# Kernel tuning notes

Hardware: AMD Instinct MI355X
Metric: run time of the kernel (lower is better)

The kernel has to match this reference:

```python
import jax, jax.numpy as jnp
import numpy as np

N, E, DIN, DOUT = 30000, 480000, 512, 512


def setup_inputs() -> dict:
    key = jax.random.key(0)
    ks = jax.random.split(key, 20)
    inp = {}
    inp["x"] = jax.random.normal(ks[0], (N, DIN), jnp.float32)
    inp["edge_index"] = jax.random.randint(ks[1], (2, E), 0, N, dtype=jnp.int64)
    inp["edge_weight"] = jax.random.uniform(ks[2], (E,), jnp.float32)
    sc = 1.0 / np.sqrt(DIN)
    sl = 1.0 / np.sqrt(2 * DOUT)
    for i, g in enumerate(["i", "f", "g", "o"]):
        inp[f"Wc_{g}"] = jax.random.normal(ks[3 + 4 * i], (DIN, DOUT), jnp.float32) * sc
        inp[f"bc_{g}"] = jnp.zeros((DOUT,), jnp.float32)
        inp[f"Wl_{g}"] = jax.random.normal(ks[4 + 4 * i], (2 * DOUT, DOUT), jnp.float32) * sl
        inp[f"bl_{g}"] = jnp.zeros((DOUT,), jnp.float32)
    return inp


def _gcn_norm(src, dst, w, n):
    # add self loops with weight 1.0 (improved=False), then symmetric normalization
    loops = jnp.arange(n, dtype=src.dtype)
    src = jnp.concatenate([src, loops])
    dst = jnp.concatenate([dst, loops])
    w = jnp.concatenate([w, jnp.ones((n,), w.dtype)])
    deg = jax.ops.segment_sum(w, dst, num_segments=n)
    dinv = jnp.where(deg > 0, jax.lax.rsqrt(jnp.where(deg > 0, deg, 1.0)), 0.0)
    norm = dinv[src] * w * dinv[dst]
    return src, dst, norm


def reference(x, edge_index, edge_weight,
              Wc_i, bc_i, Wl_i, bl_i,
              Wc_f, bc_f, Wl_f, bl_f,
              Wc_g, bc_g, Wl_g, bl_g,
              Wc_o, bc_o, Wl_o, bl_o):
    n = x.shape[0]
    src, dst, norm = _gcn_norm(edge_index[0], edge_index[1], edge_weight, n)
    H = jnp.zeros((n, DOUT), x.dtype)  # _set_hidden_state default
    C = jnp.zeros((n, DOUT), x.dtype)  # _set_cell_state default

    def conv(Wc, bc):
        xw = x @ Wc                                        # [N, DOUT] dense GEMM
        agg = jax.ops.segment_sum(norm[:, None] * xw[src], dst, num_segments=n)
        return agg + bc

    def gate(Wc, bc, Wl, bl, act):
        z = jnp.concatenate([conv(Wc, bc), H], axis=1)      # [N, 2*DOUT]
        return act(z @ Wl + bl)

    I = gate(Wc_i, bc_i, Wl_i, bl_i, jax.nn.sigmoid)
    F = gate(Wc_f, bc_f, Wl_f, bl_f, jax.nn.sigmoid)
    G = gate(Wc_g, bc_g, Wl_g, bl_g, jnp.tanh)
    O = gate(Wc_o, bc_o, Wl_o, bl_o, jax.nn.sigmoid)
    Cn = F * C + I * G
    Hn = O * jnp.tanh(Cn)
    return O, Hn, Cn
```

## Files before the change

kernel.cpp:

```cpp
#include <hip/hip_runtime.h>
#include <stdint.h>

typedef __bf16 bf16;
typedef __attribute__((ext_vector_type(4))) float f4;
typedef __attribute__((ext_vector_type(4))) float f32x4;
typedef __attribute__((ext_vector_type(8))) __bf16 bf8v;
typedef __attribute__((ext_vector_type(4))) __bf16 bf4v;

#define NN 30000
#define MPAD 30080
#define OUTSTRIDE 15360000
#define SC_B 1875

typedef __attribute__((address_space(3))) unsigned int as3_u32;
typedef __attribute__((address_space(1))) unsigned int as1_u32;

__device__ __forceinline__ void gl_lds16(const void* g, void* l) {
  __builtin_amdgcn_global_load_lds((as1_u32*)g, (as3_u32*)l, 16, 0, 0);
}

__global__ void k_pre(const int* __restrict__ ei, const float* __restrict__ ew,
                      void* __restrict__ degcnt, int E) {
  int e = blockIdx.x * 256 + threadIdx.x;
  if (e < E) {
    int d = ei[E + e];
    atomicAdd((float*)degcnt + 2 * d, ew[e]);
    atomicAdd((int*)degcnt + 2 * d + 1, 1);
  }
}

__global__ void k_bsum(const void* __restrict__ degcnt, int* __restrict__ bsum,
                       float* __restrict__ dinv, int n) {
  __shared__ int sm[256];
  int i = blockIdx.x * 256 + threadIdx.x;
  int cnt = 0;
  if (i < n) {
    int2 p = ((const int2*)degcnt)[i];
    cnt = p.y;
    dinv[i] = rsqrtf(__int_as_float(p.x) + 1.0f);
  }
  sm[threadIdx.x] = cnt;
  __syncthreads();
  for (int st = 128; st > 0; st >>= 1) {
    if (threadIdx.x < st) sm[threadIdx.x] += sm[threadIdx.x + st];
    __syncthreads();
  }
  if (threadIdx.x == 0) bsum[blockIdx.x] = sm[0];
}

__global__ void k_bscan(int* bsum, int nb) {
  __shared__ int buf[128];
  int t = threadIdx.x;
  int v = (t < nb) ? bsum[t] : 0;
  buf[t] = v;
  __syncthreads();
  for (int s = 1; s < 128; s <<= 1) {
    int u = (t >= s) ? buf[t - s] : 0;
    __syncthreads();
    buf[t] += u;
    __syncthreads();
  }
  if (t < nb) bsum[t] = buf[t] - v;
}

__global__ void k_offs(const void* __restrict__ degcnt, const int* __restrict__ bsum,
                       int* __restrict__ offs, int n, int E) {
  __shared__ int buf[256];
  int i = blockIdx.x * 256 + threadIdx.x;
  int v = (i < n) ? ((const int*)degcnt)[2 * i + 1] : 0;
  buf[threadIdx.x] = v;
  __syncthreads();
  for (int s = 1; s < 256; s <<= 1) {
    int u = (threadIdx.x >= s) ? buf[threadIdx.x - s] : 0;
    __syncthreads();
    buf[threadIdx.x] += u;
    __syncthreads();
  }
  if (i < n) offs[i] = bsum[blockIdx.x] + buf[threadIdx.x] - v;
  if (i == 0) offs[n] = E;
}

__global__ void k_xbf(const float* __restrict__ x, bf16* __restrict__ xbf, int n8) {
  int i = blockIdx.x * 256 + threadIdx.x;
  if (i >= n8) return;
  const f4* x4 = (const f4*)x;
  f4 a = x4[2 * i], b = x4[2 * i + 1];
  bf8v o;
#pragma unroll
  for (int j = 0; j < 4; ++j) { o[j] = (bf16)a[j]; o[4 + j] = (bf16)b[j]; }
  ((bf8v*)xbf)[i] = o;
}

__global__ void k_fused(const int* __restrict__ ei, const float* __restrict__ ew,
                        const float* __restrict__ dinv, const int* __restrict__ offs,
                        int* __restrict__ cursor, int2* __restrict__ sn, int E,
                        const float* __restrict__ WcA, const float* __restrict__ WlA,
                        const float* __restrict__ WcB, const float* __restrict__ WlB,
                        const float* __restrict__ WcC, const float* __restrict__ WlC,
                        bf16* __restrict__ Wt,
                        const float* __restrict__ bcA, const float* __restrict__ blA,
                        const float* __restrict__ bcB, const float* __restrict__ blB,
                        const float* __restrict__ bcC, const float* __restrict__ blC,
                        float* __restrict__ bcomb) {
  __shared__ float sWc[64][17];
  __shared__ float sWl[16][64];
  __shared__ float smr[4][64];
  int b = blockIdx.x;
  if (b < SC_B) {
    int e = b * 256 + threadIdx.x;
    if (e >= E) return;
    int s = ei[e], d = ei[E + e];
    int pos = offs[d] + atomicAdd(&cursor[d], 1);
    sn[pos] = make_int2(s, __float_as_int(dinv[s] * ew[e] * dinv[d]));
  } else if (b < SC_B + 192) {
    int bb = b - SC_B;
    int g = bb >> 6, rem = bb & 63;
    const float* Wc; const float* Wl;
    if (g == 0)      { Wc = WcA; Wl = WlA; }
    else if (g == 1) { Wc = WcB; Wl = WlB; }
    else             { Wc = WcC; Wl = WlC; }
    int k0 = (rem & 7) * 64, j0 = (rem >> 3) * 64;
    int t = threadIdx.x, tx = t & 15, ty = t >> 4;
    float acc[4][4] = {};
    for (int c0 = 0; c0 < 512; c0 += 16) {
      { int kk = t >> 2, c4 = (t & 3) * 4;
        f4 v = *(const f4*)(Wc + (size_t)(k0 + kk) * 512 + c0 + c4);
#pragma unroll
        for (int j = 0; j < 4; ++j) sWc[kk][c4 + j] = v[j]; }
      { int cc = t >> 4, j4 = (t & 15) * 4;
        f4 v = *(const f4*)(Wl + (size_t)(c0 + cc) * 512 + j0 + j4);
        *(f4*)&sWl[cc][j4] = v; }
      __syncthreads();
#pragma unroll
      for (int cc = 0; cc < 16; ++cc) {
        float wcv[4], wlv[4];
#pragma unroll
        for (int q = 0; q < 4; ++q) wcv[q] = sWc[tx * 4 + q][cc];
#pragma unroll
        for (int a = 0; a < 4; ++a) wlv[a] = sWl[cc][ty * 4 + a];
#pragma unroll
        for (int a = 0; a < 4; ++a)
#pragma unroll
          for (int q = 0; q < 4; ++q) acc[a][q] += wlv[a] * wcv[q];
      }
      __syncthreads();
    }
#pragma unroll
    for (int a = 0; a < 4; ++a) {
      bf4v o;
#pragma unroll
      for (int q = 0; q < 4; ++q) o[q] = (bf16)acc[a][q];
      *(bf4v*)&Wt[((size_t)g * 512 + j0 + ty * 4 + a) * 512 + k0 + tx * 4] = o;
    }
  } else {
    int bb = b - SC_B - 192;
    int g = bb >> 3, jc = bb & 7;
    const float* bc; const float* bl; const float* Wl;
    if (g == 0)      { bc = bcA; bl = blA; Wl = WlA; }
    else if (g == 1) { bc = bcB; bl = blB; Wl = WlB; }
    else             { bc = bcC; bl = blC; Wl = WlC; }
    int jl = threadIdx.x & 63, part = threadIdx.x >> 6;
    int j = jc * 64 + jl;
    float s = 0.f;
    for (int c = part * 128; c < part * 128 + 128; ++c)
      s += bc[c] * Wl[(size_t)c * 512 + j];
    smr[part][jl] = s;
    __syncthreads();
    if (part == 0)
      bcomb[g * 512 + j] = bl[j] + smr[0][jl] + smr[1][jl] + smr[2][jl] + smr[3][jl];
  }
}

__global__ __launch_bounds__(256) void k_agg(const int* __restrict__ offs, const int2* __restrict__ sn,
                                             const float* __restrict__ dinv, const bf16* __restrict__ xbf,
                                             bf16* __restrict__ ybf) {
  int wv = (blockIdx.x * 256 + threadIdx.x) >> 6;
  int lane = threadIdx.x & 63;
  if (wv >= MPAD) return;
  bf16* yrow = ybf + ((size_t)wv << 9) + lane * 8;
  if (wv >= NN) {
    bf8v z;
#pragma unroll
    for (int j = 0; j < 8; ++j) z[j] = (bf16)0.f;
    *(bf8v*)yrow = z;
    return;
  }
  float acc[8];
  float s0 = dinv[wv]; s0 *= s0;
  bf8v xv0 = *(const bf8v*)(xbf + ((size_t)wv << 9) + lane * 8);
#pragma unroll
  for (int j = 0; j < 8; ++j) acc[j] = s0 * (float)xv0[j];
  int e = offs[wv], end = offs[wv + 1];
  int2 p0, p1, p2, p3;
  const bool have = (e + 4 <= end);
  if (have) { p0 = sn[e]; p1 = sn[e + 1]; p2 = sn[e + 2]; p3 = sn[e + 3]; }
  for (; e + 8 <= end; e += 4) {
    int2 q0 = sn[e + 4], q1 = sn[e + 5], q2 = sn[e + 6], q3 = sn[e + 7];
    bf8v v0 = *(const bf8v*)(xbf + ((size_t)p0.x << 9) + lane * 8);
    bf8v v1 = *(const bf8v*)(xbf + ((size_t)p1.x << 9) + lane * 8);
    bf8v v2 = *(const bf8v*)(xbf + ((size_t)p2.x << 9) + lane * 8);
    bf8v v3 = *(const bf8v*)(xbf + ((size_t)p3.x << 9) + lane * 8);
    float n0 = __int_as_float(p0.y), n1 = __int_as_float(p1.y);
    float n2 = __int_as_float(p2.y), n3 = __int_as_float(p3.y);
#pragma unroll
    for (int j = 0; j < 8; ++j)
      acc[j] += n0 * (float)v0[j] + n1 * (float)v1[j] + n2 * (float)v2[j] + n3 * (float)v3[j];
    p0 = q0; p1 = q1; p2 = q2; p3 = q3;
  }
  if (have) {
    bf8v v0 = *(const bf8v*)(xbf + ((size_t)p0.x << 9) + lane * 8);
    bf8v v1 = *(const bf8v*)(xbf + ((size_t)p1.x << 9) + lane * 8);
    bf8v v2 = *(const bf8v*)(xbf + ((size_t)p2.x << 9) + lane * 8);
    bf8v v3 = *(const bf8v*)(xbf + ((size_t)p3.x << 9) + lane * 8);
    float n0 = __int_as_float(p0.y), n1 = __int_as_float(p1.y);
    float n2 = __int_as_float(p2.y), n3 = __int_as_float(p3.y);
#pragma unroll
    for (int j = 0; j < 8; ++j)
      acc[j] += n0 * (float)v0[j] + n1 * (float)v1[j] + n2 * (float)v2[j] + n3 * (float)v3[j];
    e += 4;
  }
  for (; e < end; ++e) {
    int2 p = sn[e];
    bf8v v = *(const bf8v*)(xbf + ((size_t)p.x << 9) + lane * 8);
    float nn = __int_as_float(p.y);
#pragma unroll
    for (int j = 0; j < 8; ++j) acc[j] += nn * (float)v[j];
  }
  bf8v o;
#pragma unroll
  for (int j = 0; j < 8; ++j) o[j] = (bf16)acc[j];
  *(bf8v*)yrow = o;
}

__global__ __launch_bounds__(256, 4) void k_gemm(const bf16* __restrict__ A, const bf16* __restrict__ Bt,
                                                 const float* __restrict__ bcomb, float* __restrict__ out) {
  __shared__ __align__(16) char lds[32768];
  const int t = threadIdx.x, lane = t & 63, w = t >> 6;
  const int wm = w >> 1, wn = w & 1;
  const int d = blockIdx.x;
  const int s = (d & 7) * 470 + (d >> 3);
  const int m0 = (s >> 3) * 64, n0 = (s & 7) * 64;
  const int l15 = lane & 15, lhi = lane >> 4;
  f32x4 acc[3][2][2] = {};

  const int lq = lane >> 2;
  const int sw = (lane >> 3) & 3;
  const int kcol = 16 * ((lane & 3) ^ sw);
  const int rswz = 16 * (lhi ^ ((l15 >> 1) & 3));

  const char* aS = (const char*)A + ((size_t)(m0 + w * 16 + lq) << 10) + kcol;
  const char* bS[3];
#pragma unroll
  for (int i = 0; i < 3; ++i) {
    int bi = i * 4 + w, g = bi >> 2, q = bi & 3;
    bS[i] = (const char*)Bt + ((size_t)(g * 512 + n0 + q * 16 + lq) << 10) + kcol;
  }
  const int vA = (wm * 32 + l15) * 64 + rswz;
  const int vB = 4096 + (wn * 32 + l15) * 64 + rswz;

  auto stage = [&](int bufoff, int kp) {
    gl_lds16(aS + kp * 64, lds + bufoff + w * 1024 + lane * 16);
#pragma unroll
    for (int i = 0; i < 3; ++i)
      gl_lds16(bS[i] + kp * 64, lds + bufoff + 4096 + (i * 4 + w) * 1024 + lane * 16);
  };

  auto compute = [&](int bufoff) {
    bf8v af[2];
#pragma unroll
    for (int mi = 0; mi < 2; ++mi)
      af[mi] = *(const bf8v*)(lds + bufoff + vA + mi * 1024);
#pragma unroll
    for (int g = 0; g < 3; ++g) {
      bf8v b0 = *(const bf8v*)(lds + bufoff + vB + g * 4096);
      bf8v b1 = *(const bf8v*)(lds + bufoff + vB + g * 4096 + 1024);
#pragma unroll
      for (int mi = 0; mi < 2; ++mi) {
        acc[g][mi][0] = __builtin_amdgcn_mfma_f32_16x16x32_bf16(b0, af[mi], acc[g][mi][0], 0, 0, 0);
        acc[g][mi][1] = __builtin_amdgcn_mfma_f32_16x16x32_bf16(b1, af[mi], acc[g][mi][1], 0, 0, 0);
      }
    }
  };

  stage(0, 0);
  stage(16384, 1);
#pragma unroll
  for (int kp = 0; kp < 16; ++kp) {
    if (kp < 15) asm volatile("s_waitcnt vmcnt(4)" ::: "memory");
    else         asm volatile("s_waitcnt vmcnt(0)" ::: "memory");
    __builtin_amdgcn_sched_barrier(0);
    __builtin_amdgcn_s_barrier();
    __builtin_amdgcn_sched_barrier(0);
    compute((kp & 1) * 16384);
    __builtin_amdgcn_sched_barrier(0);
    __builtin_amdgcn_s_barrier();
    __builtin_amdgcn_sched_barrier(0);
    if (kp < 14) stage((kp & 1) * 16384, kp + 2);
  }

#pragma unroll
  for (int ni = 0; ni < 2; ++ni) {
    int nb = n0 + wn * 32 + ni * 16 + lhi * 4;
    f4 bI = *(const f4*)&bcomb[nb];
    f4 bG = *(const f4*)&bcomb[512 + nb];
    f4 bO = *(const f4*)&bcomb[1024 + nb];
#pragma unroll
    for (int mi = 0; mi < 2; ++mi) {
      int row = m0 + wm * 32 + mi * 16 + l15;
      if (row < NN) {
        f4 vO, vH, vC;
#pragma unroll
        for (int r = 0; r < 4; ++r) {
          float zi = acc[0][mi][ni][r] + bI[r];
          float zg = acc[1][mi][ni][r] + bG[r];
          float zo = acc[2][mi][ni][r] + bO[r];
          float I = 1.f / (1.f + __expf(-zi));
          float e2g = __expf(2.f * zg);
          float G = (e2g - 1.f) / (e2g + 1.f);
          float O = 1.f / (1.f + __expf(-zo));
          float Cn = I * G;
          float e2c = __expf(2.f * Cn);
          float tc = (e2c - 1.f) / (e2c + 1.f);
          vO[r] = O; vH[r] = O * tc; vC[r] = Cn;
        }
        size_t base = ((size_t)row << 9) + nb;
        __builtin_nontemporal_store(vO, (f4*)&out[base]);
        __builtin_nontemporal_store(vH, (f4*)&out[OUTSTRIDE + base]);
        __builtin_nontemporal_store(vC, (f4*)&out[2 * OUTSTRIDE + base]);
      }
    }
  }
}

extern "C" void kernel_launch(void* const* d_in, const int* in_sizes, int n_in,
                              void* d_out, int out_size, void* d_ws, size_t ws_size,
                              hipStream_t stream) {
  const float* x   = (const float*)d_in[0];
  const int*   ei  = (const int*)d_in[1];
  const float* ew  = (const float*)d_in[2];
  const float* Wc_i = (const float*)d_in[3];
  const float* bc_i = (const float*)d_in[4];
  const float* Wl_i = (const float*)d_in[5];
  const float* bl_i = (const float*)d_in[6];
  const float* Wc_g = (const float*)d_in[11];
  const float* bc_g = (const float*)d_in[12];
  const float* Wl_g = (const float*)d_in[13];
  const float* bl_g = (const float*)d_in[14];
  const float* Wc_o = (const float*)d_in[15];
  const float* bc_o = (const float*)d_in[16];
  const float* Wl_o = (const float*)d_in[17];
  const float* bl_o = (const float*)d_in[18];

  const int E = in_sizes[2];
  const int n = in_sizes[0] / 512;
  const int NB = (n + 255) / 256;

  char* ws = (char*)d_ws;
  bf16*  ybf   = (bf16*)ws;
  float* dinv  = (float*)(ws + 30801920);
  bf16*  Wt    = (bf16*)(ws + 30924800);
  float* bcomb = (float*)(ws + 32497664);
  int*   bsum  = (int*)(ws + 32503808);
  (void)ws_size;

  char* ob = (char*)d_out;
  float* out    = (float*)d_out;
  bf16*  xbf    = (bf16*)ob;
  int2*  sn     = (int2*)(ob + 30720000);
  void*  degcnt = (void*)(ob + 34560000);
  int*   curs   = (int*)(ob + 34800000);
  int*   offs   = (int*)(ob + 34920000);
  (void)out_size; (void)n_in;

  hipMemsetAsync(degcnt, 0, 360000, stream);
  k_xbf<<<(n * 512 / 8 + 255) / 256, 256, 0, stream>>>(x, xbf, n * 512 / 8);
  k_pre<<<(E + 255) / 256, 256, 0, stream>>>(ei, ew, degcnt, E);
  k_bsum<<<NB, 256, 0, stream>>>(degcnt, bsum, dinv, n);
  k_bscan<<<1, 128, 0, stream>>>(bsum, NB);
  k_offs<<<NB, 256, 0, stream>>>(degcnt, bsum, offs, n, E);
  k_fused<<<SC_B + 192 + 24, 256, 0, stream>>>(ei, ew, dinv, offs, curs, sn, E,
                                               Wc_i, Wl_i, Wc_g, Wl_g, Wc_o, Wl_o, Wt,
                                               bc_i, bl_i, bc_g, bl_g, bc_o, bl_o, bcomb);
  k_agg<<<(MPAD * 64 + 255) / 256, 256, 0, stream>>>(offs, sn, dinv, xbf, ybf);
  k_gemm<<<3760, 256, 0, stream>>>(ybf, Wt, bcomb, out);
}
```

Before: 303.8 us.

## Fuse CSR preprocessing into fewer launches with packed double atomics and atomic offsets

After: 279.1 us. 8.1% less time.

```diff
diff --git a/kernel.cpp b/kernel.cpp
--- a/kernel.cpp
+++ b/kernel.cpp
@@ -10,7 +10,9 @@
 #define NN 30000
 #define MPAD 30080
 #define OUTSTRIDE 15360000
+#define XB 7500
 #define SC_B 1875
+#define TWO32 4294967296.0
 
 typedef __attribute__((address_space(3))) unsigned int as3_u32;
 typedef __attribute__((address_space(1))) unsigned int as1_u32;
@@ -19,80 +21,42 @@
   __builtin_amdgcn_global_load_lds((as1_u32*)g, (as3_u32*)l, 16, 0, 0);
 }
 
-__global__ void k_pre(const int* __restrict__ ei, const float* __restrict__ ew,
-                      void* __restrict__ degcnt, int E) {
-  int e = blockIdx.x * 256 + threadIdx.x;
-  if (e < E) {
-    int d = ei[E + e];
-    atomicAdd((float*)degcnt + 2 * d, ew[e]);
-    atomicAdd((int*)degcnt + 2 * d + 1, 1);
-  }
-}
-
-__global__ void k_bsum(const void* __restrict__ degcnt, int* __restrict__ bsum,
-                       float* __restrict__ dinv, int n) {
-  __shared__ int sm[256];
+__global__ void k_xp(const float* __restrict__ x, bf16* __restrict__ xbf,
+                     const int* __restrict__ ei, const float* __restrict__ ew,
+                     double* __restrict__ degcnt, int E) {
+  int b = blockIdx.x;
+  if (b < XB) {
+    int i = b * 256 + threadIdx.x;
+    const f4* x4 = (const f4*)x;
+    f4 a = x4[2 * i], c = x4[2 * i + 1];
+    bf8v o;
+#pragma unroll
+    for (int j = 0; j < 4; ++j) { o[j] = (bf16)a[j]; o[4 + j] = (bf16)c[j]; }
+    ((bf8v*)xbf)[i] = o;
+  } else {
+    int e = (b - XB) * 256 + threadIdx.x;
+    if (e < E) {
+      int d = ei[E + e];
+      atomicAdd(&degcnt[d], (double)ew[e] + TWO32);
+    }
+  }
+}
+
+__global__ void k_doffs(const double* __restrict__ degcnt, float* __restrict__ dinv,
+                        int* __restrict__ gctr, int2* __restrict__ off2, int n) {
   int i = blockIdx.x * 256 + threadIdx.x;
-  int cnt = 0;
-  if (i < n) {
-    int2 p = ((const int2*)degcnt)[i];
-    cnt = p.y;
-    dinv[i] = rsqrtf(__int_as_float(p.x) + 1.0f);
-  }
-  sm[threadIdx.x] = cnt;
-  __syncthreads();
-  for (int st = 128; st > 0; st >>= 1) {
-    if (threadIdx.x < st) sm[threadIdx.x] += sm[threadIdx.x + st];
-    __syncthreads();
-  }
-  if (threadIdx.x == 0) bsum[blockIdx.x] = sm[0];
-}
-
-__global__ void k_bscan(int* bsum, int nb) {
-  __shared__ int buf[128];
-  int t = threadIdx.x;
-  int v = (t < nb) ? bsum[t] : 0;
-  buf[t] = v;
-  __syncthreads();
-  for (int s = 1; s < 128; s <<= 1) {
-    int u = (t >= s) ? buf[t - s] : 0;
-    __syncthreads();
-    buf[t] += u;
-    __syncthreads();
-  }
-  if (t < nb) bsum[t] = buf[t] - v;
-}
-
-__global__ void k_offs(const void* __restrict__ degcnt, const int* __restrict__ bsum,
-                       int* __restrict__ offs, int n, int E) {
-  __shared__ int buf[256];
-  int i = blockIdx.x * 256 + threadIdx.x;
-  int v = (i < n) ? ((const int*)degcnt)[2 * i + 1] : 0;
-  buf[threadIdx.x] = v;
-  __syncthreads();
-  for (int s = 1; s < 256; s <<= 1) {
-    int u = (threadIdx.x >= s) ? buf[threadIdx.x - s] : 0;
-    __syncthreads();
-    buf[threadIdx.x] += u;
-    __syncthreads();
-  }
-  if (i < n) offs[i] = bsum[blockIdx.x] + buf[threadIdx.x] - v;
-  if (i == 0) offs[n] = E;
-}
-
-__global__ void k_xbf(const float* __restrict__ x, bf16* __restrict__ xbf, int n8) {
-  int i = blockIdx.x * 256 + threadIdx.x;
-  if (i >= n8) return;
-  const f4* x4 = (const f4*)x;
-  f4 a = x4[2 * i], b = x4[2 * i + 1];
-  bf8v o;
-#pragma unroll
-  for (int j = 0; j < 4; ++j) { o[j] = (bf16)a[j]; o[4 + j] = (bf16)b[j]; }
-  ((bf8v*)xbf)[i] = o;
+  if (i >= n) return;
+  double v = degcnt[i];
+  double c = (double)(long long)(v * (1.0 / TWO32));
+  int cnt = (int)c;
+  float deg = (float)(v - c * TWO32);
+  dinv[i] = rsqrtf(deg + 1.0f);
+  int start = atomicAdd(gctr, cnt);
+  off2[i] = make_int2(start, start + cnt);
 }
 
 __global__ void k_fused(const int* __restrict__ ei, const float* __restrict__ ew,
-                        const float* __restrict__ dinv, const int* __restrict__ offs,
+                        const float* __restrict__ dinv, const int2* __restrict__ off2,
                         int* __restrict__ cursor, int2* __restrict__ sn, int E,
                         const float* __restrict__ WcA, const float* __restrict__ WlA,
                         const float* __restrict__ WcB, const float* __restrict__ WlB,
@@ -110,7 +74,7 @@
     int e = b * 256 + threadIdx.x;
     if (e >= E) return;
     int s = ei[e], d = ei[E + e];
-    int pos = offs[d] + atomicAdd(&cursor[d], 1);
+    int pos = off2[d].x + atomicAdd(&cursor[d], 1);
     sn[pos] = make_int2(s, __float_as_int(dinv[s] * ew[e] * dinv[d]));
   } else if (b < SC_B + 192) {
     int bb = b - SC_B;
@@ -171,7 +135,7 @@
   }
 }
 
-__global__ __launch_bounds__(256) void k_agg(const int* __restrict__ offs, const int2* __restrict__ sn,
+__global__ __launch_bounds__(256) void k_agg(const int2* __restrict__ off2, const int2* __restrict__ sn,
                                              const float* __restrict__ dinv, const bf16* __restrict__ xbf,
                                              bf16* __restrict__ ybf) {
   int wv = (blockIdx.x * 256 + threadIdx.x) >> 6;
@@ -190,7 +154,8 @@
   bf8v xv0 = *(const bf8v*)(xbf + ((size_t)wv << 9) + lane * 8);
 #pragma unroll
   for (int j = 0; j < 8; ++j) acc[j] = s0 * (float)xv0[j];
-  int e = offs[wv], end = offs[wv + 1];
+  int2 seg = off2[wv];
+  int e = seg.x, end = seg.y;
   int2 p0, p1, p2, p3;
   const bool have = (e + 4 <= end);
   if (have) { p0 = sn[e]; p1 = sn[e + 1]; p2 = sn[e + 2]; p3 = sn[e + 3]; }
@@ -232,7 +197,7 @@
   *(bf8v*)yrow = o;
 }
 
-__global__ __launch_bounds__(256, 4) void k_gemm(const bf16* __restrict__ A, const bf16* __restrict__ Bt,
+__global__ __launch_bounds__(256, 5) void k_gemm(const bf16* __restrict__ A, const bf16* __restrict__ Bt,
                                                  const float* __restrict__ bcomb, float* __restrict__ out) {
   __shared__ __align__(16) char lds[32768];
   const int t = threadIdx.x, lane = t & 63, w = t >> 6;
@@ -360,27 +325,24 @@
   float* dinv  = (float*)(ws + 30801920);
   bf16*  Wt    = (bf16*)(ws + 30924800);
   float* bcomb = (float*)(ws + 32497664);
-  int*   bsum  = (int*)(ws + 32503808);
   (void)ws_size;
 
   char* ob = (char*)d_out;
-  float* out    = (float*)d_out;
-  bf16*  xbf    = (bf16*)ob;
-  int2*  sn     = (int2*)(ob + 30720000);
-  void*  degcnt = (void*)(ob + 34560000);
-  int*   curs   = (int*)(ob + 34800000);
-  int*   offs   = (int*)(ob + 34920000);
+  float*  out    = (float*)d_out;
+  bf16*   xbf    = (bf16*)ob;
+  int2*   sn     = (int2*)(ob + 30720000);
+  double* degcnt = (double*)(ob + 34560000);
+  int*    curs   = (int*)(ob + 34800000);
+  int*    gctr   = (int*)(ob + 34920000);
+  int2*   off2   = (int2*)(ob + 34920064);
   (void)out_size; (void)n_in;
 
-  hipMemsetAsync(degcnt, 0, 360000, stream);
-  k_xbf<<<(n * 512 / 8 + 255) / 256, 256, 0, stream>>>(x, xbf, n * 512 / 8);
-  k_pre<<<(E + 255) / 256, 256, 0, stream>>>(ei, ew, degcnt, E);
-  k_bsum<<<NB, 256, 0, stream>>>(degcnt, bsum, dinv, n);
-  k_bscan<<<1, 128, 0, stream>>>(bsum, NB);
-  k_offs<<<NB, 256, 0, stream>>>(degcnt, bsum, offs, n, E);
-  k_fused<<<SC_B + 192 + 24, 256, 0, stream>>>(ei, ew, dinv, offs, curs, sn, E,
+  hipMemsetAsync(degcnt, 0, 360064, stream);
+  k_xp<<<XB + (E + 255) / 256, 256, 0, stream>>>(x, xbf, ei, ew, degcnt, E);
+  k_doffs<<<NB, 256, 0, stream>>>(degcnt, dinv, gctr, off2, n);
+  k_fused<<<SC_B + 192 + 24, 256, 0, stream>>>(ei, ew, dinv, off2, curs, sn, E,
                                                Wc_i, Wl_i, Wc_g, Wl_g, Wc_o, Wl_o, Wt,
                                                bc_i, bl_i, bc_g, bl_g, bc_o, bl_o, bcomb);
-  k_agg<<<(MPAD * 64 + 255) / 256, 256, 0, stream>>>(offs, sn, dinv, xbf, ybf);
+  k_agg<<<(MPAD * 64 + 255) / 256, 256, 0, stream>>>(off2, sn, dinv, xbf, ybf);
   k_gemm<<<3760, 256, 0, stream>>>(ybf, Wt, bcomb, out);
 }
```
